# Kernel optimization log

Hardware: AMD Instinct MI355X
Metric: run time of the kernel (lower is better)

Reference implementation:

```python
import jax, jax.numpy as jnp
import numpy as np

B, S, D, E, K = 2, 2048, 512, 8, 2
H = 4 * D  # 2048


def setup_inputs() -> dict:
    key = jax.random.key(0)
    ks = jax.random.split(key, 6)
    x = jax.random.normal(ks[0], (B, S, D), dtype=jnp.float32)
    # parameters, matching torch init (randn weights, zero biases)
    w1 = jax.random.normal(ks[1], (E, D, H), dtype=jnp.float32)
    w2 = jax.random.normal(ks[2], (E, H, D), dtype=jnp.float32)
    b1 = jnp.zeros((E, H), dtype=jnp.float32)
    b2 = jnp.zeros((E, D), dtype=jnp.float32)
    # nn.Linear(D, E): kaiming-uniform-ish; plain uniform is fine for a baseline
    lim = 1.0 / np.sqrt(D)
    router_w = jax.random.uniform(ks[3], (D, E), dtype=jnp.float32, minval=-lim, maxval=lim)
    router_b = jax.random.uniform(ks[4], (E,), dtype=jnp.float32, minval=-lim, maxval=lim)
    return {"x": x, "w1": w1, "w2": w2, "b1": b1, "b2": b2,
            "router_w": router_w, "router_b": router_b}


def reference(x, w1, w2, b1, b2, router_w, router_b):
    # router: [b,s,e]
    router_logits = jnp.einsum('bsd,de->bse', x, router_w) + router_b
    top_k_logits, top_k_indices = jax.lax.top_k(router_logits, K)   # [b,s,k]
    top_k_probs = jax.nn.softmax(top_k_logits, axis=-1)             # [b,s,k]
    masks = jax.nn.one_hot(top_k_indices, E, dtype=x.dtype)          # [b,s,k,e]
    # dense all-expert MLP (faithful to source: every expert on every token)
    h = jnp.einsum('bsd,edh->bseh', x, w1) + b1                      # [b,s,e,4d]
    h = jax.nn.gelu(h, approximate=False)                            # exact gelu
    y = jnp.einsum('bseh,ehd->bsed', h, w2) + b2                     # [b,s,e,d]
    # combine: mask each expert output by routed prob and sum over top-k
    out = jnp.einsum('bsed,bske,bsk->bsd', y, masks, top_k_probs)    # [b,s,d]
    return out
```

## Files before the change

kernel.cpp:

```cpp
#include <hip/hip_runtime.h>
#include <math.h>

typedef unsigned short u16;
typedef __bf16 bf16x8 __attribute__((ext_vector_type(8)));
typedef float f32x4 __attribute__((ext_vector_type(4)));

#define T_TOKENS 4096
#define D_DIM    512
#define H_DIM    2048
#define E_NUM    8
#define CAP      4096
#define NSLOT    (T_TOKENS * 2)
#define NCHUNK   16

__device__ __forceinline__ u16 f2bf(float f) {
  unsigned int u = __builtin_bit_cast(unsigned int, f);
  u = (u + 0x7fffu + ((u >> 16) & 1u)) >> 16;
  return (u16)u;
}

__device__ __forceinline__ void gload16(const void* g, void* l) {
  __builtin_amdgcn_global_load_lds(
      (__attribute__((address_space(1))) void*)(g),
      (__attribute__((address_space(3))) void*)(l), 16, 0, 0);
}

__device__ __forceinline__ float gelu_fast(float v) {
  float u = v * __fmaf_rn(0.071354817f, v * v, 1.59576912f);
  float e = __expf(-u);
  return v * __builtin_amdgcn_rcpf(1.0f + e);
}

__global__ __launch_bounds__(256) void transpose_both_kernel(const float* __restrict__ w1,
                                                             const float* __restrict__ w2,
                                                             u16* __restrict__ w1t,
                                                             u16* __restrict__ w2t) {
  __shared__ float tile[64][67];
  int bid = blockIdx.x;
  const float* in; u16* out; int R, C;
  if (bid < 2048) { in = w1; out = w1t; R = D_DIM; C = H_DIM; }
  else            { bid -= 2048; in = w2; out = w2t; R = H_DIM; C = D_DIM; }
  const int e = bid >> 8;
  const int t = bid & 255;
  const int nCx = C >> 6;
  const int c0 = (t % nCx) * 64, r0 = (t / nCx) * 64;
  const float* src = in + (size_t)e * D_DIM * H_DIM;
  u16* dst = out + (size_t)e * D_DIM * H_DIM;
  const int tid = threadIdx.x;
  {
    const int row = tid >> 2, cc = (tid & 3) * 16;
    const float* s = src + (size_t)(r0 + row) * C + c0 + cc;
#pragma unroll
    for (int j = 0; j < 4; j++)
      *(float4*)(&tile[row][cc + 4 * j]) = *(const float4*)(s + 4 * j);
  }
  __syncthreads();
  {
    const int c = tid >> 2, rc = (tid & 3) * 16;
    u16 buf[16];
#pragma unroll
    for (int j = 0; j < 16; j++) buf[j] = f2bf(tile[rc + j][c]);
    u16* d = dst + (size_t)(c0 + c) * R + r0 + rc;
    *(uint4*)(d)     = *(uint4*)(&buf[0]);
    *(uint4*)(d + 8) = *(uint4*)(&buf[8]);
  }
}

__global__ __launch_bounds__(256) void router_kernel(const float* __restrict__ x,
                                                     const float* __restrict__ rw,
                                                     const float* __restrict__ rb,
                                                     int* __restrict__ topk_idx,
                                                     float* __restrict__ topk_p,
                                                     u16* __restrict__ xb,
                                                     float* __restrict__ outz) {
  {
    float4 z = {0.f, 0.f, 0.f, 0.f};
    float4* o = (float4*)(outz + (size_t)blockIdx.x * 2048);
    o[threadIdx.x] = z;
    o[threadIdx.x + 256] = z;
  }
  const int lane = threadIdx.x & 63;
  const int t = blockIdx.x * 4 + (threadIdx.x >> 6);
  const float* xr = x + (size_t)t * D_DIM + lane * 8;
  float xv[8];
  *(float4*)(&xv[0]) = *(const float4*)(xr);
  *(float4*)(&xv[4]) = *(const float4*)(xr + 4);
  ushort4 o0, o1;
  o0.x = f2bf(xv[0]); o0.y = f2bf(xv[1]); o0.z = f2bf(xv[2]); o0.w = f2bf(xv[3]);
  o1.x = f2bf(xv[4]); o1.y = f2bf(xv[5]); o1.z = f2bf(xv[6]); o1.w = f2bf(xv[7]);
  ushort4* xo = (ushort4*)(xb + (size_t)t * D_DIM + lane * 8);
  xo[0] = o0; xo[1] = o1;

  float acc[8] = {0.f,0.f,0.f,0.f,0.f,0.f,0.f,0.f};
#pragma unroll
  for (int j = 0; j < 8; j++) {
    const float4* w = (const float4*)(rw + (size_t)(lane * 8 + j) * E_NUM);
    float4 w0 = w[0], w1 = w[1];
    acc[0] += xv[j] * w0.x; acc[1] += xv[j] * w0.y;
    acc[2] += xv[j] * w0.z; acc[3] += xv[j] * w0.w;
    acc[4] += xv[j] * w1.x; acc[5] += xv[j] * w1.y;
    acc[6] += xv[j] * w1.z; acc[7] += xv[j] * w1.w;
  }
#pragma unroll
  for (int off = 32; off > 0; off >>= 1) {
#pragma unroll
    for (int e = 0; e < 8; e++) acc[e] += __shfl_down(acc[e], off);
  }
  if (lane == 0) {
    float l[8];
#pragma unroll
    for (int e = 0; e < 8; e++) l[e] = acc[e] + rb[e];
    int i0 = 0; float v0 = l[0];
#pragma unroll
    for (int e = 1; e < 8; e++) if (l[e] > v0) { v0 = l[e]; i0 = e; }
    int i1 = -1; float v1 = -3.4e38f;
#pragma unroll
    for (int e = 0; e < 8; e++) if (e != i0 && l[e] > v1) { v1 = l[e]; i1 = e; }
    float p1 = expf(v1 - v0);
    float s = 1.0f + p1;
    topk_idx[t * 2] = i0; topk_idx[t * 2 + 1] = i1;
    topk_p[t * 2] = 1.0f / s; topk_p[t * 2 + 1] = p1 / s;
  }
}

__global__ __launch_bounds__(256) void count_kernel(const int* __restrict__ topk_idx,
                                                    int* __restrict__ chunkcnt) {
  const int b = blockIdx.x, tid = threadIdx.x, lane = tid & 63, w = tid >> 6;
  const int t = b * 256 + tid;
  const int i0 = topk_idx[t * 2], i1 = topk_idx[t * 2 + 1];
  __shared__ int ws[4][E_NUM];
#pragma unroll
  for (int e = 0; e < E_NUM; e++) {
    unsigned long long m = __ballot(i0 == e || i1 == e);
    if (lane == 0) ws[w][e] = (int)__popcll(m);
  }
  __syncthreads();
  if (tid < E_NUM)
    chunkcnt[b * E_NUM + tid] = ws[0][tid] + ws[1][tid] + ws[2][tid] + ws[3][tid];
}

__global__ __launch_bounds__(256) void scatter_kernel(const int* __restrict__ topk_idx,
                                                      const float* __restrict__ topk_p,
                                                      const int* __restrict__ chunkcnt,
                                                      int* __restrict__ slot_list,
                                                      float* __restrict__ prob_list,
                                                      int* __restrict__ counts) {
  const int e = blockIdx.x & 7, chunk = blockIdx.x >> 3;
  const int tid = threadIdx.x, lane = tid & 63, w = tid >> 6;
  int base = 0;
  for (int c = 0; c < chunk; ++c) base += chunkcnt[c * E_NUM + e];
  const int t = chunk * 256 + tid;
  const int i0 = topk_idx[t * 2], i1 = topk_idx[t * 2 + 1];
  int flag = 0, slot = 0; float p = 0.f;
  if (i0 == e)      { flag = 1; slot = t * 2;     p = topk_p[t * 2]; }
  else if (i1 == e) { flag = 1; slot = t * 2 + 1; p = topk_p[t * 2 + 1]; }
  unsigned long long m = __ballot(flag);
  __shared__ int wsum[4];
  if (lane == 0) wsum[w] = (int)__popcll(m);
  const int wpre = (int)__popcll(m & ((1ull << lane) - 1ull));
  __syncthreads();
  int wb = base;
#pragma unroll
  for (int j = 0; j < 4; j++) if (j < w) wb += wsum[j];
  if (flag) { slot_list[e * CAP + wb + wpre] = slot; prob_list[e * CAP + wb + wpre] = p; }
  if (chunk == NCHUNK - 1 && tid == 0)
    counts[e] = base + wsum[0] + wsum[1] + wsum[2] + wsum[3];
}

__global__ __launch_bounds__(256, 3) void gemm1_kernel(const u16* __restrict__ xb,
                                                       const u16* __restrict__ w1t,
                                                       const float* __restrict__ b1,
                                                       const int* __restrict__ slot_list,
                                                       const float* __restrict__ prob_list,
                                                       const int* __restrict__ counts,
                                                       u16* __restrict__ hbuf) {
  const int e  = blockIdx.y >> 6;
  const int rt = blockIdx.y & 63;
  const int cnt = counts[e];
  const int rbase = rt * 64;
  if (rbase >= cnt) return;
  const int n0 = blockIdx.x * 128;

  __shared__ __align__(16) u16 At[2][64 * 64];
  __shared__ __align__(16) u16 Bt[2][128 * 64];

  const int tid = threadIdx.x, lane = tid & 63, wid = tid >> 6;
  const int wr = wid >> 1, wc = wid & 1;
  const int lr8 = lane >> 3;
  const int sx = lane & 7;
  const int kperm = (sx ^ lr8) * 8;
  const int lrow = lane & 15, lk = lane >> 4;

  const u16* pa[2]; int loa[2];
#pragma unroll
  for (int i = 0; i < 2; i++) {
    const int row = (wid * 2 + i) * 8 + lr8;
    const int grow = rbase + row;
    int tok = 0;
    if (grow < cnt) tok = slot_list[e * CAP + grow] >> 1;
    pa[i] = xb + (size_t)tok * D_DIM + kperm;
    loa[i] = (wid * 2 + i) * 512;
  }
  const u16* pb[4]; int lob[4];
#pragma unroll
  for (int i = 0; i < 4; i++) {
    const int row = (wid * 4 + i) * 8 + lr8;
    pb[i] = w1t + ((size_t)e * H_DIM + n0 + row) * D_DIM + kperm;
    lob[i] = (wid * 4 + i) * 512;
  }

  f32x4 acc[2][4];
#pragma unroll
  for (int i = 0; i < 2; i++)
#pragma unroll
    for (int j = 0; j < 4; j++) acc[i][j] = (f32x4){0.f, 0.f, 0.f, 0.f};

  auto stage = [&](int k0, int b) {
#pragma unroll
    for (int i = 0; i < 2; i++) gload16(pa[i] + k0, &At[b][loa[i]]);
#pragma unroll
    for (int i = 0; i < 4; i++) gload16(pb[i] + k0, &Bt[b][lob[i]]);
  };

  stage(0, 0);
  const int nt = D_DIM / 64;
  int cur = 0;
  for (int t = 0; t < nt; ++t) {
    asm volatile("s_waitcnt vmcnt(0)" ::: "memory");
    __builtin_amdgcn_sched_barrier(0);
    __builtin_amdgcn_s_barrier();
    if (t + 1 < nt) stage((t + 1) * 64, cur ^ 1);
    bf16x8 afr[2][2], bfr[4][2];
#pragma unroll
    for (int ks = 0; ks < 2; ks++) {
#pragma unroll
      for (int fq = 0; fq < 2; fq++)
        afr[fq][ks] = *(const bf16x8*)(&At[cur][(wr * 32 + fq * 16 + lrow) * 64 + ((ks * 4 + lk) ^ sx) * 8]);
#pragma unroll
      for (int fq = 0; fq < 4; fq++)
        bfr[fq][ks] = *(const bf16x8*)(&Bt[cur][(wc * 64 + fq * 16 + lrow) * 64 + ((ks * 4 + lk) ^ sx) * 8]);
    }
    asm volatile("s_waitcnt lgkmcnt(0)" ::: "memory");
    __builtin_amdgcn_sched_barrier(0);
    __builtin_amdgcn_s_setprio(1);
#pragma unroll
    for (int ks = 0; ks < 2; ks++)
#pragma unroll
      for (int fr = 0; fr < 2; fr++)
#pragma unroll
        for (int fc = 0; fc < 4; fc++)
          acc[fr][fc] = __builtin_amdgcn_mfma_f32_16x16x32_bf16(afr[fr][ks], bfr[fc][ks], acc[fr][fc], 0, 0, 0);
    __builtin_amdgcn_s_setprio(0);
    cur ^= 1;
  }

  float bias[4];
#pragma unroll
  for (int fc = 0; fc < 4; fc++) bias[fc] = b1[e * H_DIM + n0 + wc * 64 + fc * 16 + lrow];
#pragma unroll
  for (int fr = 0; fr < 2; fr++) {
#pragma unroll
    for (int reg = 0; reg < 4; reg++) {
      const int rloc = wr * 32 + fr * 16 + lk * 4 + reg;
      const int grow = rbase + rloc;
      if (grow < cnt) {
        const int slot = slot_list[e * CAP + grow];
        const float p  = prob_list[e * CAP + grow];
        u16* dst = hbuf + (size_t)slot * H_DIM + n0 + wc * 64 + lrow;
#pragma unroll
        for (int fc = 0; fc < 4; fc++) {
          float v = acc[fr][fc][reg] + bias[fc];
          dst[fc * 16] = f2bf(gelu_fast(v) * p);
        }
      }
    }
  }
}

__global__ __launch_bounds__(256, 3) void gemm2_kernel(const u16* __restrict__ hbuf,
                                                       const u16* __restrict__ w2t,
                                                       const float* __restrict__ b2,
                                                       const int* __restrict__ slot_list,
                                                       const float* __restrict__ prob_list,
                                                       const int* __restrict__ counts,
                                                       float* __restrict__ out) {
  const int e  = blockIdx.y >> 6;
  const int rt = blockIdx.y & 63;
  const int cnt = counts[e];
  const int rbase = rt * 64;
  if (rbase >= cnt) return;
  const int n0 = blockIdx.x * 128;

  __shared__ __align__(16) u16 At[2][64 * 64];
  __shared__ __align__(16) u16 Bt[2][128 * 64];

  const int tid = threadIdx.x, lane = tid & 63, wid = tid >> 6;
  const int wr = wid >> 1, wc = wid & 1;
  const int lr8 = lane >> 3;
  const int sx = lane & 7;
  const int kperm = (sx ^ lr8) * 8;
  const int lrow = lane & 15, lk = lane >> 4;

  const u16* pa[2]; int loa[2];
#pragma unroll
  for (int i = 0; i < 2; i++) {
    const int row = (wid * 2 + i) * 8 + lr8;
    const int grow = rbase + row;
    int slot = 0;
    if (grow < cnt) slot = slot_list[e * CAP + grow];
    pa[i] = hbuf + (size_t)slot * H_DIM + kperm;
    loa[i] = (wid * 2 + i) * 512;
  }
  const u16* pb[4]; int lob[4];
#pragma unroll
  for (int i = 0; i < 4; i++) {
    const int row = (wid * 4 + i) * 8 + lr8;
    pb[i] = w2t + ((size_t)e * D_DIM + n0 + row) * H_DIM + kperm;
    lob[i] = (wid * 4 + i) * 512;
  }

  f32x4 acc[2][4];
#pragma unroll
  for (int i = 0; i < 2; i++)
#pragma unroll
    for (int j = 0; j < 4; j++) acc[i][j] = (f32x4){0.f, 0.f, 0.f, 0.f};

  auto stage = [&](int k0, int b) {
#pragma unroll
    for (int i = 0; i < 2; i++) gload16(pa[i] + k0, &At[b][loa[i]]);
#pragma unroll
    for (int i = 0; i < 4; i++) gload16(pb[i] + k0, &Bt[b][lob[i]]);
  };

  stage(0, 0);
  const int nt = H_DIM / 64;
  int cur = 0;
  for (int t = 0; t < nt; ++t) {
    asm volatile("s_waitcnt vmcnt(0)" ::: "memory");
    __builtin_amdgcn_sched_barrier(0);
    __builtin_amdgcn_s_barrier();
    if (t + 1 < nt) stage((t + 1) * 64, cur ^ 1);
    bf16x8 afr[2][2], bfr[4][2];
#pragma unroll
    for (int ks = 0; ks < 2; ks++) {
#pragma unroll
      for (int fq = 0; fq < 2; fq++)
        afr[fq][ks] = *(const bf16x8*)(&At[cur][(wr * 32 + fq * 16 + lrow) * 64 + ((ks * 4 + lk) ^ sx) * 8]);
#pragma unroll
      for (int fq = 0; fq < 4; fq++)
        bfr[fq][ks] = *(const bf16x8*)(&Bt[cur][(wc * 64 + fq * 16 + lrow) * 64 + ((ks * 4 + lk) ^ sx) * 8]);
    }
    asm volatile("s_waitcnt lgkmcnt(0)" ::: "memory");
    __builtin_amdgcn_sched_barrier(0);
    __builtin_amdgcn_s_setprio(1);
#pragma unroll
    for (int ks = 0; ks < 2; ks++)
#pragma unroll
      for (int fr = 0; fr < 2; fr++)
#pragma unroll
        for (int fc = 0; fc < 4; fc++)
          acc[fr][fc] = __builtin_amdgcn_mfma_f32_16x16x32_bf16(afr[fr][ks], bfr[fc][ks], acc[fr][fc], 0, 0, 0);
    __builtin_amdgcn_s_setprio(0);
    cur ^= 1;
  }

#pragma unroll
  for (int fr = 0; fr < 2; fr++) {
#pragma unroll
    for (int reg = 0; reg < 4; reg++) {
      const int rloc = wr * 32 + fr * 16 + lk * 4 + reg;
      const int grow = rbase + rloc;
      if (grow < cnt) {
        const int slot = slot_list[e * CAP + grow];
        const float p  = prob_list[e * CAP + grow];
        float* dst = out + (size_t)(slot >> 1) * D_DIM + n0 + wc * 64 + lrow;
#pragma unroll
        for (int fc = 0; fc < 4; fc++) {
          float v = acc[fr][fc][reg] + p * b2[e * D_DIM + n0 + wc * 64 + fc * 16 + lrow];
          atomicAdd(&dst[fc * 16], v);
        }
      }
    }
  }
}

extern "C" void kernel_launch(void* const* d_in, const int* in_sizes, int n_in,
                              void* d_out, int out_size, void* d_ws, size_t ws_size,
                              hipStream_t stream) {
  const float* x  = (const float*)d_in[0];
  const float* w1 = (const float*)d_in[1];
  const float* w2 = (const float*)d_in[2];
  const float* b1 = (const float*)d_in[3];
  const float* b2 = (const float*)d_in[4];
  const float* rw = (const float*)d_in[5];
  const float* rb = (const float*)d_in[6];
  float* out = (float*)d_out;

  char* ws = (char*)d_ws;
  size_t off = 0;
  auto alloc = [&](size_t bytes) -> void* {
    void* p = ws + off;
    off = (off + bytes + 255) & ~(size_t)255;
    return p;
  };
  int*   counts    = (int*)alloc(E_NUM * 4);
  int*   chunkcnt  = (int*)alloc(NCHUNK * E_NUM * 4);
  int*   slot_list = (int*)alloc((size_t)E_NUM * CAP * 4);
  float* prob_list = (float*)alloc((size_t)E_NUM * CAP * 4);
  int*   topk_idx  = (int*)alloc((size_t)T_TOKENS * 2 * 4);
  float* topk_p    = (float*)alloc((size_t)T_TOKENS * 2 * 4);
  u16*   xb        = (u16*)alloc((size_t)T_TOKENS * D_DIM * 2);
  u16*   w1t       = (u16*)alloc((size_t)E_NUM * H_DIM * D_DIM * 2);
  u16*   w2t       = (u16*)alloc((size_t)E_NUM * H_DIM * D_DIM * 2);
  u16*   hbuf      = (u16*)alloc((size_t)NSLOT * H_DIM * 2);

  transpose_both_kernel<<<4096, 256, 0, stream>>>(w1, w2, w1t, w2t);
  router_kernel<<<T_TOKENS / 4, 256, 0, stream>>>(x, rw, rb, topk_idx, topk_p, xb, out);
  count_kernel<<<NCHUNK, 256, 0, stream>>>(topk_idx, chunkcnt);
  scatter_kernel<<<NCHUNK * E_NUM, 256, 0, stream>>>(topk_idx, topk_p, chunkcnt, slot_list, prob_list, counts);
  gemm1_kernel<<<dim3(16, E_NUM * 64), 256, 0, stream>>>(xb, w1t, b1, slot_list, prob_list, counts, hbuf);
  gemm2_kernel<<<dim3(4, E_NUM * 64), 256, 0, stream>>>(hbuf, w2t, b2, slot_list, prob_list, counts, out);
}
```

Before: 120.0 us.

## Deepen GEMM pipelines to four stages with BK=32 and enlarge gemm1 tile

Result: slower. 142.6 us (+18.8%).

```diff
diff --git a/kernel.cpp b/kernel.cpp
--- a/kernel.cpp
+++ b/kernel.cpp
@@ -167,110 +167,112 @@
     counts[e] = base + wsum[0] + wsum[1] + wsum[2] + wsum[3];
 }
 
-__global__ __launch_bounds__(256, 3) void gemm1_kernel(const u16* __restrict__ xb,
+__global__ __launch_bounds__(256, 2) void gemm1_kernel(const u16* __restrict__ xb,
                                                        const u16* __restrict__ w1t,
                                                        const float* __restrict__ b1,
                                                        const int* __restrict__ slot_list,
                                                        const float* __restrict__ prob_list,
                                                        const int* __restrict__ counts,
                                                        u16* __restrict__ hbuf) {
-  const int e  = blockIdx.y >> 6;
-  const int rt = blockIdx.y & 63;
+  const int e  = blockIdx.y >> 5;
+  const int rt = blockIdx.y & 31;
   const int cnt = counts[e];
-  const int rbase = rt * 64;
+  const int rbase = rt * 128;
   if (rbase >= cnt) return;
   const int n0 = blockIdx.x * 128;
 
-  __shared__ __align__(16) u16 At[2][64 * 64];
-  __shared__ __align__(16) u16 Bt[2][128 * 64];
+  __shared__ __align__(16) u16 At[4][128 * 32];
+  __shared__ __align__(16) u16 Bt[4][128 * 32];
 
   const int tid = threadIdx.x, lane = tid & 63, wid = tid >> 6;
   const int wr = wid >> 1, wc = wid & 1;
-  const int lr8 = lane >> 3;
-  const int sx = lane & 7;
-  const int kperm = (sx ^ lr8) * 8;
   const int lrow = lane & 15, lk = lane >> 4;
 
-  const u16* pa[2]; int loa[2];
+  const u16* pa[2]; const u16* pb[2]; int lo[2];
 #pragma unroll
   for (int i = 0; i < 2; i++) {
-    const int row = (wid * 2 + i) * 8 + lr8;
+    const int g = (wid * 2 + i) * 64 + lane;
+    const int row = g >> 2, c = g & 3;
+    const int sxk = (row >> 1) & 3;
+    const int coff = (c ^ sxk) << 3;
     const int grow = rbase + row;
     int tok = 0;
     if (grow < cnt) tok = slot_list[e * CAP + grow] >> 1;
-    pa[i] = xb + (size_t)tok * D_DIM + kperm;
-    loa[i] = (wid * 2 + i) * 512;
-  }
-  const u16* pb[4]; int lob[4];
-#pragma unroll
-  for (int i = 0; i < 4; i++) {
-    const int row = (wid * 4 + i) * 8 + lr8;
-    pb[i] = w1t + ((size_t)e * H_DIM + n0 + row) * D_DIM + kperm;
-    lob[i] = (wid * 4 + i) * 512;
-  }
-
-  f32x4 acc[2][4];
-#pragma unroll
-  for (int i = 0; i < 2; i++)
+    pa[i] = xb + (size_t)tok * D_DIM + coff;
+    pb[i] = w1t + ((size_t)e * H_DIM + n0 + row) * D_DIM + coff;
+    lo[i] = (wid * 2 + i) * 512;
+  }
+
+  int aoff[4], boff[4];
+#pragma unroll
+  for (int f = 0; f < 4; f++) {
+    const int ra = wr * 64 + f * 16 + lrow;
+    aoff[f] = ra * 32 + ((lk ^ ((ra >> 1) & 3)) << 3);
+    const int rb_ = wc * 64 + f * 16 + lrow;
+    boff[f] = rb_ * 32 + ((lk ^ ((rb_ >> 1) & 3)) << 3);
+  }
+
+  f32x4 acc[4][4];
+#pragma unroll
+  for (int i = 0; i < 4; i++)
 #pragma unroll
     for (int j = 0; j < 4; j++) acc[i][j] = (f32x4){0.f, 0.f, 0.f, 0.f};
 
-  auto stage = [&](int k0, int b) {
-#pragma unroll
-    for (int i = 0; i < 2; i++) gload16(pa[i] + k0, &At[b][loa[i]]);
-#pragma unroll
-    for (int i = 0; i < 4; i++) gload16(pb[i] + k0, &Bt[b][lob[i]]);
+  auto stage = [&](int t) {
+    const int s = t & 3;
+    const int k0 = t * 32;
+#pragma unroll
+    for (int i = 0; i < 2; i++) gload16(pa[i] + k0, &At[s][lo[i]]);
+#pragma unroll
+    for (int i = 0; i < 2; i++) gload16(pb[i] + k0, &Bt[s][lo[i]]);
   };
 
-  stage(0, 0);
-  const int nt = D_DIM / 64;
-  int cur = 0;
+  const int nt = D_DIM / 32;
+  stage(0); stage(1); stage(2);
   for (int t = 0; t < nt; ++t) {
-    asm volatile("s_waitcnt vmcnt(0)" ::: "memory");
+    const int fl = nt - 1 - t;
+    if (fl >= 2)      { asm volatile("s_waitcnt vmcnt(8)" ::: "memory"); }
+    else if (fl == 1) { asm volatile("s_waitcnt vmcnt(4)" ::: "memory"); }
+    else              { asm volatile("s_waitcnt vmcnt(0)" ::: "memory"); }
     __builtin_amdgcn_sched_barrier(0);
     __builtin_amdgcn_s_barrier();
-    if (t + 1 < nt) stage((t + 1) * 64, cur ^ 1);
-    bf16x8 afr[2][2], bfr[4][2];
-#pragma unroll
-    for (int ks = 0; ks < 2; ks++) {
-#pragma unroll
-      for (int fq = 0; fq < 2; fq++)
-        afr[fq][ks] = *(const bf16x8*)(&At[cur][(wr * 32 + fq * 16 + lrow) * 64 + ((ks * 4 + lk) ^ sx) * 8]);
-#pragma unroll
-      for (int fq = 0; fq < 4; fq++)
-        bfr[fq][ks] = *(const bf16x8*)(&Bt[cur][(wc * 64 + fq * 16 + lrow) * 64 + ((ks * 4 + lk) ^ sx) * 8]);
+    __builtin_amdgcn_sched_barrier(0);
+    if (t + 3 < nt) stage(t + 3);
+    const int s = t & 3;
+    bf16x8 afr[4], bfr[4];
+#pragma unroll
+    for (int f = 0; f < 4; f++) {
+      afr[f] = *(const bf16x8*)(&At[s][aoff[f]]);
+      bfr[f] = *(const bf16x8*)(&Bt[s][boff[f]]);
     }
     asm volatile("s_waitcnt lgkmcnt(0)" ::: "memory");
     __builtin_amdgcn_sched_barrier(0);
     __builtin_amdgcn_s_setprio(1);
 #pragma unroll
-    for (int ks = 0; ks < 2; ks++)
-#pragma unroll
-      for (int fr = 0; fr < 2; fr++)
-#pragma unroll
-        for (int fc = 0; fc < 4; fc++)
-          acc[fr][fc] = __builtin_amdgcn_mfma_f32_16x16x32_bf16(afr[fr][ks], bfr[fc][ks], acc[fr][fc], 0, 0, 0);
+    for (int fm = 0; fm < 4; fm++)
+#pragma unroll
+      for (int fn = 0; fn < 4; fn++)
+        acc[fm][fn] = __builtin_amdgcn_mfma_f32_16x16x32_bf16(afr[fm], bfr[fn], acc[fm][fn], 0, 0, 0);
     __builtin_amdgcn_s_setprio(0);
-    cur ^= 1;
   }
 
   float bias[4];
 #pragma unroll
-  for (int fc = 0; fc < 4; fc++) bias[fc] = b1[e * H_DIM + n0 + wc * 64 + fc * 16 + lrow];
-#pragma unroll
-  for (int fr = 0; fr < 2; fr++) {
+  for (int fn = 0; fn < 4; fn++) bias[fn] = b1[e * H_DIM + n0 + wc * 64 + fn * 16 + lrow];
+#pragma unroll
+  for (int fm = 0; fm < 4; fm++) {
 #pragma unroll
     for (int reg = 0; reg < 4; reg++) {
-      const int rloc = wr * 32 + fr * 16 + lk * 4 + reg;
+      const int rloc = wr * 64 + fm * 16 + lk * 4 + reg;
       const int grow = rbase + rloc;
       if (grow < cnt) {
         const int slot = slot_list[e * CAP + grow];
         const float p  = prob_list[e * CAP + grow];
         u16* dst = hbuf + (size_t)slot * H_DIM + n0 + wc * 64 + lrow;
 #pragma unroll
-        for (int fc = 0; fc < 4; fc++) {
-          float v = acc[fr][fc][reg] + bias[fc];
-          dst[fc * 16] = f2bf(gelu_fast(v) * p);
+        for (int fn = 0; fn < 4; fn++) {
+          float v = acc[fm][fn][reg] + bias[fn];
+          dst[fn * 16] = f2bf(gelu_fast(v) * p);
         }
       }
     }
@@ -291,32 +293,46 @@
   if (rbase >= cnt) return;
   const int n0 = blockIdx.x * 128;
 
-  __shared__ __align__(16) u16 At[2][64 * 64];
-  __shared__ __align__(16) u16 Bt[2][128 * 64];
+  __shared__ __align__(16) u16 At[4][64 * 32];
+  __shared__ __align__(16) u16 Bt[4][128 * 32];
 
   const int tid = threadIdx.x, lane = tid & 63, wid = tid >> 6;
   const int wr = wid >> 1, wc = wid & 1;
-  const int lr8 = lane >> 3;
-  const int sx = lane & 7;
-  const int kperm = (sx ^ lr8) * 8;
   const int lrow = lane & 15, lk = lane >> 4;
 
-  const u16* pa[2]; int loa[2];
-#pragma unroll
-  for (int i = 0; i < 2; i++) {
-    const int row = (wid * 2 + i) * 8 + lr8;
+  const u16* pa; int loa;
+  {
+    const int g = wid * 64 + lane;
+    const int row = g >> 2, c = g & 3;
+    const int sxk = (row >> 1) & 3;
+    const int coff = (c ^ sxk) << 3;
     const int grow = rbase + row;
     int slot = 0;
     if (grow < cnt) slot = slot_list[e * CAP + grow];
-    pa[i] = hbuf + (size_t)slot * H_DIM + kperm;
-    loa[i] = (wid * 2 + i) * 512;
-  }
-  const u16* pb[4]; int lob[4];
-#pragma unroll
-  for (int i = 0; i < 4; i++) {
-    const int row = (wid * 4 + i) * 8 + lr8;
-    pb[i] = w2t + ((size_t)e * D_DIM + n0 + row) * H_DIM + kperm;
-    lob[i] = (wid * 4 + i) * 512;
+    pa = hbuf + (size_t)slot * H_DIM + coff;
+    loa = wid * 512;
+  }
+  const u16* pb[2]; int lob[2];
+#pragma unroll
+  for (int i = 0; i < 2; i++) {
+    const int g = (wid * 2 + i) * 64 + lane;
+    const int row = g >> 2, c = g & 3;
+    const int sxk = (row >> 1) & 3;
+    const int coff = (c ^ sxk) << 3;
+    pb[i] = w2t + ((size_t)e * D_DIM + n0 + row) * H_DIM + coff;
+    lob[i] = (wid * 2 + i) * 512;
+  }
+
+  int aoff[2], boff[4];
+#pragma unroll
+  for (int f = 0; f < 2; f++) {
+    const int ra = wr * 32 + f * 16 + lrow;
+    aoff[f] = ra * 32 + ((lk ^ ((ra >> 1) & 3)) << 3);
+  }
+#pragma unroll
+  for (int f = 0; f < 4; f++) {
+    const int rb_ = wc * 64 + f * 16 + lrow;
+    boff[f] = rb_ * 32 + ((lk ^ ((rb_ >> 1) & 3)) << 3);
   }
 
   f32x4 acc[2][4];
@@ -325,59 +341,56 @@
 #pragma unroll
     for (int j = 0; j < 4; j++) acc[i][j] = (f32x4){0.f, 0.f, 0.f, 0.f};
 
-  auto stage = [&](int k0, int b) {
-#pragma unroll
-    for (int i = 0; i < 2; i++) gload16(pa[i] + k0, &At[b][loa[i]]);
-#pragma unroll
-    for (int i = 0; i < 4; i++) gload16(pb[i] + k0, &Bt[b][lob[i]]);
+  auto stage = [&](int t) {
+    const int s = t & 3;
+    const int k0 = t * 32;
+    gload16(pa + k0, &At[s][loa]);
+#pragma unroll
+    for (int i = 0; i < 2; i++) gload16(pb[i] + k0, &Bt[s][lob[i]]);
   };
 
-  stage(0, 0);
-  const int nt = H_DIM / 64;
-  int cur = 0;
+  const int nt = H_DIM / 32;
+  stage(0); stage(1); stage(2);
   for (int t = 0; t < nt; ++t) {
-    asm volatile("s_waitcnt vmcnt(0)" ::: "memory");
+    const int fl = nt - 1 - t;
+    if (fl >= 2)      { asm volatile("s_waitcnt vmcnt(6)" ::: "memory"); }
+    else if (fl == 1) { asm volatile("s_waitcnt vmcnt(3)" ::: "memory"); }
+    else              { asm volatile("s_waitcnt vmcnt(0)" ::: "memory"); }
     __builtin_amdgcn_sched_barrier(0);
     __builtin_amdgcn_s_barrier();
-    if (t + 1 < nt) stage((t + 1) * 64, cur ^ 1);
-    bf16x8 afr[2][2], bfr[4][2];
-#pragma unroll
-    for (int ks = 0; ks < 2; ks++) {
-#pragma unroll
-      for (int fq = 0; fq < 2; fq++)
-        afr[fq][ks] = *(const bf16x8*)(&At[cur][(wr * 32 + fq * 16 + lrow) * 64 + ((ks * 4 + lk) ^ sx) * 8]);
-#pragma unroll
-      for (int fq = 0; fq < 4; fq++)
-        bfr[fq][ks] = *(const bf16x8*)(&Bt[cur][(wc * 64 + fq * 16 + lrow) * 64 + ((ks * 4 + lk) ^ sx) * 8]);
-    }
+    __builtin_amdgcn_sched_barrier(0);
+    if (t + 3 < nt) stage(t + 3);
+    const int s = t & 3;
+    bf16x8 afr[2], bfr[4];
+#pragma unroll
+    for (int f = 0; f < 2; f++) afr[f] = *(const bf16x8*)(&At[s][aoff[f]]);
+#pragma unroll
+    for (int f = 0; f < 4; f++) bfr[f] = *(const bf16x8*)(&Bt[s][boff[f]]);
     asm volatile("s_waitcnt lgkmcnt(0)" ::: "memory");
     __builtin_amdgcn_sched_barrier(0);
     __builtin_amdgcn_s_setprio(1);
 #pragma unroll
-    for (int ks = 0; ks < 2; ks++)
-#pragma unroll
-      for (int fr = 0; fr < 2; fr++)
-#pragma unroll
-        for (int fc = 0; fc < 4; fc++)
-          acc[fr][fc] = __builtin_amdgcn_mfma_f32_16x16x32_bf16(afr[fr][ks], bfr[fc][ks], acc[fr][fc], 0, 0, 0);
+    for (int fm = 0; fm < 2; fm++)
+#pragma unroll
+      for (int fn = 0; fn < 4; fn++)
+        acc[fm][fn] = __builtin_amdgcn_mfma_f32_16x16x32_bf16(afr[fm], bfr[fn], acc[fm][fn], 0, 0, 0);
     __builtin_amdgcn_s_setprio(0);
-    cur ^= 1;
-  }
-
-#pragma unroll
-  for (int fr = 0; fr < 2; fr++) {
+  }
+
+#pragma unroll
+  for (int fm = 0; fm < 2; fm++) {
 #pragma unroll
     for (int reg = 0; reg < 4; reg++) {
-      const int rloc = wr * 32 + fr * 16 + lk * 4 + reg;
+      const int rloc = wr * 32 + fm * 16 + lk * 4 + reg;
       const int grow = rbase + rloc;
       if (grow < cnt) {
         const int slot = slot_list[e * CAP + grow];
         const float p  = prob_list[e * CAP + grow];
         float* dst = out + (size_t)(slot >> 1) * D_DIM + n0 + wc * 64 + lrow;
 #pragma unroll
-        for (int fc = 0; fc < 4; fc++) {
-          float v = acc[fr][fc][reg] + p * b2[e * D_DIM + n0 + wc * 64 + fc * 16 + lrow];
-          atomicAdd(&dst[fc * 16], v);
+        for (int fn = 0; fn < 4; fn++) {
+          float v = acc[fm][fn][reg] + p * b2[e * D_DIM + n0 + wc * 64 + fn * 16 + lrow];
+          atomicAdd(&dst[fn * 16], v);
         }
       }
     }
@@ -418,6 +431,6 @@
   router_kernel<<<T_TOKENS / 4, 256, 0, stream>>>(x, rw, rb, topk_idx, topk_p, xb, out);
   count_kernel<<<NCHUNK, 256, 0, stream>>>(topk_idx, chunkcnt);
   scatter_kernel<<<NCHUNK * E_NUM, 256, 0, stream>>>(topk_idx, topk_p, chunkcnt, slot_list, prob_list, counts);
-  gemm1_kernel<<<dim3(16, E_NUM * 64), 256, 0, stream>>>(xb, w1t, b1, slot_list, prob_list, counts, hbuf);
+  gemm1_kernel<<<dim3(16, E_NUM * 32), 256, 0, stream>>>(xb, w1t, b1, slot_list, prob_list, counts, hbuf);
   gemm2_kernel<<<dim3(4, E_NUM * 64), 256, 0, stream>>>(hbuf, w2t, b2, slot_list, prob_list, counts, out);
 }
```

## Compact hidden buffer per expert, interleave experts in grid, split-K gemm2

Applied to the files above, without the earlier changes.

Measured after the change: 125.0 us. +4.1%, slower.

```diff
diff --git a/kernel.cpp b/kernel.cpp
--- a/kernel.cpp
+++ b/kernel.cpp
@@ -173,13 +173,18 @@
                                                        const int* __restrict__ slot_list,
                                                        const float* __restrict__ prob_list,
                                                        const int* __restrict__ counts,
-                                                       u16* __restrict__ hbuf) {
-  const int e  = blockIdx.y >> 6;
-  const int rt = blockIdx.y & 63;
+                                                       u16* __restrict__ hbufc) {
+  const int e  = blockIdx.x & 7;
+  const int g  = blockIdx.x >> 3;
+  const int cx = g & 15;
+  const int rt = g >> 4;
   const int cnt = counts[e];
   const int rbase = rt * 64;
   if (rbase >= cnt) return;
-  const int n0 = blockIdx.x * 128;
+  int ebase = 0;
+#pragma unroll
+  for (int j = 0; j < E_NUM; j++) if (j < e) ebase += counts[j];
+  const int n0 = cx * 128;
 
   __shared__ __align__(16) u16 At[2][64 * 64];
   __shared__ __align__(16) u16 Bt[2][128 * 64];
@@ -264,9 +269,8 @@
       const int rloc = wr * 32 + fr * 16 + lk * 4 + reg;
       const int grow = rbase + rloc;
       if (grow < cnt) {
-        const int slot = slot_list[e * CAP + grow];
-        const float p  = prob_list[e * CAP + grow];
-        u16* dst = hbuf + (size_t)slot * H_DIM + n0 + wc * 64 + lrow;
+        const float p = prob_list[e * CAP + grow];
+        u16* dst = hbufc + (size_t)(ebase + grow) * H_DIM + n0 + wc * 64 + lrow;
 #pragma unroll
         for (int fc = 0; fc < 4; fc++) {
           float v = acc[fr][fc][reg] + bias[fc];
@@ -277,19 +281,26 @@
   }
 }
 
-__global__ __launch_bounds__(256, 3) void gemm2_kernel(const u16* __restrict__ hbuf,
+__global__ __launch_bounds__(256, 3) void gemm2_kernel(const u16* __restrict__ hbufc,
                                                        const u16* __restrict__ w2t,
                                                        const float* __restrict__ b2,
                                                        const int* __restrict__ slot_list,
                                                        const float* __restrict__ prob_list,
                                                        const int* __restrict__ counts,
                                                        float* __restrict__ out) {
-  const int e  = blockIdx.y >> 6;
-  const int rt = blockIdx.y & 63;
+  const int e  = blockIdx.x & 7;
+  const int g  = blockIdx.x >> 3;
+  const int cx = g & 3;
+  const int s  = (g >> 2) & 1;
+  const int rt = g >> 3;
   const int cnt = counts[e];
   const int rbase = rt * 64;
   if (rbase >= cnt) return;
-  const int n0 = blockIdx.x * 128;
+  int ebase = 0;
+#pragma unroll
+  for (int j = 0; j < E_NUM; j++) if (j < e) ebase += counts[j];
+  const int n0 = cx * 128;
+  const int kb = s * (H_DIM / 2);
 
   __shared__ __align__(16) u16 At[2][64 * 64];
   __shared__ __align__(16) u16 Bt[2][128 * 64];
@@ -306,16 +317,15 @@
   for (int i = 0; i < 2; i++) {
     const int row = (wid * 2 + i) * 8 + lr8;
     const int grow = rbase + row;
-    int slot = 0;
-    if (grow < cnt) slot = slot_list[e * CAP + grow];
-    pa[i] = hbuf + (size_t)slot * H_DIM + kperm;
+    const int cr = (grow < cnt) ? (ebase + grow) : 0;
+    pa[i] = hbufc + (size_t)cr * H_DIM + kb + kperm;
     loa[i] = (wid * 2 + i) * 512;
   }
   const u16* pb[4]; int lob[4];
 #pragma unroll
   for (int i = 0; i < 4; i++) {
     const int row = (wid * 4 + i) * 8 + lr8;
-    pb[i] = w2t + ((size_t)e * D_DIM + n0 + row) * H_DIM + kperm;
+    pb[i] = w2t + ((size_t)e * D_DIM + n0 + row) * H_DIM + kb + kperm;
     lob[i] = (wid * 4 + i) * 512;
   }
 
@@ -333,7 +343,7 @@
   };
 
   stage(0, 0);
-  const int nt = H_DIM / 64;
+  const int nt = (H_DIM / 2) / 64;
   int cur = 0;
   for (int t = 0; t < nt; ++t) {
     asm volatile("s_waitcnt vmcnt(0)" ::: "memory");
@@ -376,7 +386,8 @@
         float* dst = out + (size_t)(slot >> 1) * D_DIM + n0 + wc * 64 + lrow;
 #pragma unroll
         for (int fc = 0; fc < 4; fc++) {
-          float v = acc[fr][fc][reg] + p * b2[e * D_DIM + n0 + wc * 64 + fc * 16 + lrow];
+          float v = acc[fr][fc][reg];
+          if (s == 0) v += p * b2[e * D_DIM + n0 + wc * 64 + fc * 16 + lrow];
           atomicAdd(&dst[fc * 16], v);
         }
       }
@@ -412,12 +423,12 @@
   u16*   xb        = (u16*)alloc((size_t)T_TOKENS * D_DIM * 2);
   u16*   w1t       = (u16*)alloc((size_t)E_NUM * H_DIM * D_DIM * 2);
   u16*   w2t       = (u16*)alloc((size_t)E_NUM * H_DIM * D_DIM * 2);
-  u16*   hbuf      = (u16*)alloc((size_t)NSLOT * H_DIM * 2);
+  u16*   hbufc     = (u16*)alloc((size_t)NSLOT * H_DIM * 2);
 
   transpose_both_kernel<<<4096, 256, 0, stream>>>(w1, w2, w1t, w2t);
   router_kernel<<<T_TOKENS / 4, 256, 0, stream>>>(x, rw, rb, topk_idx, topk_p, xb, out);
   count_kernel<<<NCHUNK, 256, 0, stream>>>(topk_idx, chunkcnt);
   scatter_kernel<<<NCHUNK * E_NUM, 256, 0, stream>>>(topk_idx, topk_p, chunkcnt, slot_list, prob_list, counts);
-  gemm1_kernel<<<dim3(16, E_NUM * 64), 256, 0, stream>>>(xb, w1t, b1, slot_list, prob_list, counts, hbuf);
-  gemm2_kernel<<<dim3(4, E_NUM * 64), 256, 0, stream>>>(hbuf, w2t, b2, slot_list, prob_list, counts, out);
-}
+  gemm1_kernel<<<E_NUM * 16 * 64, 256, 0, stream>>>(xb, w1t, b1, slot_list, prob_list, counts, hbufc);
+  gemm2_kernel<<<E_NUM * 4 * 2 * 64, 256, 0, stream>>>(hbufc, w2t, b2, slot_list, prob_list, counts, out);
+}
```
